# Kernel optimization log

Hardware: AMD Instinct MI355X
Metric: run time of the kernel (lower is better)

Reference implementation:

```python
import jax, jax.numpy as jnp
import numpy as np

DIST_MULT = 0.1
CLIP_LOW = 0.0
EPS = 1e-6


def setup_inputs() -> dict:
    key = jax.random.key(0)
    k1, _ = jax.random.split(key)
    x_msg_binned = jax.random.normal(k1, (8, 64, 512, 16), dtype=jnp.float32)
    msk = jnp.ones((8, 64, 512, 1), dtype=jnp.float32)
    return {"x_msg_binned": x_msg_binned, "msk": msk}


def reference(x_msg_binned, msk):
    # A: (B, bins, N, F) masked node features
    A = x_msg_binned * msk
    na = jnp.sum(A * A, axis=-1)  # (B, bins, N)
    # Gram matrix: (B, bins, N, N)
    G = jnp.einsum("bknf,bkmf->bknm", A, A)
    D = jnp.sqrt(jnp.maximum(na[..., :, None] - 2.0 * G + na[..., None, :], EPS))
    dm = jnp.exp(-DIST_MULT * D)[..., None]  # (B, bins, N, N, 1)
    return jnp.clip(dm, CLIP_LOW, 1.0)
```

## Files before the change

kernel.cpp:

```cpp
#include <hip/hip_runtime.h>


typedef float f32x4 __attribute__((ext_vector_type(4)));

#define NEG_DIST_LOG2E (-0.14426950408889634f)
#define EPS_F 1e-6f
#define LDM 516
#define LDN 68

__global__ __launch_bounds__(512) void node_pair_gaussian_kernel(
    const float* __restrict__ x,
    const float* __restrict__ msk,
    float* __restrict__ out)
{
    __shared__ __align__(16) float lds_m[16][LDM];
    __shared__ __align__(16) float lds_n[16][LDN];
    __shared__ __align__(16) float na_m[512];
    __shared__ __align__(16) float na_n[64];

    const int tid   = threadIdx.x;
    const int slice = blockIdx.x;
    const int r0    = blockIdx.y << 6;

    const float* xs = x   + (size_t)slice * (512 * 16);
    const float* ms = msk + (size_t)slice * 512;

    #pragma unroll
    for (int it = 0; it < 4; ++it) {
        const int c    = tid + it * 512;
        const int node = c >> 2;
        const int f4   = (c & 3) * 4;
        const f32x4 v  = *(const f32x4*)(xs + (size_t)c * 4);
        const float mm = ms[node];
        lds_m[f4 + 0][node] = v.x * mm;
        lds_m[f4 + 1][node] = v.y * mm;
        lds_m[f4 + 2][node] = v.z * mm;
        lds_m[f4 + 3][node] = v.w * mm;
        float p = (v.x * v.x + v.y * v.y + v.z * v.z + v.w * v.w) * (mm * mm);
        p += __shfl_xor(p, 1);
        p += __shfl_xor(p, 2);
        if ((tid & 3) == 0) na_m[node] = p;
    }
    if (tid < 256) {
        const int node = tid >> 2;
        const int f4   = (tid & 3) * 4;
        const f32x4 v  = *(const f32x4*)(xs + (size_t)(r0 + node) * 16 + f4);
        const float mm = ms[r0 + node];
        lds_n[f4 + 0][node] = v.x * mm;
        lds_n[f4 + 1][node] = v.y * mm;
        lds_n[f4 + 2][node] = v.z * mm;
        lds_n[f4 + 3][node] = v.w * mm;
        float p = (v.x * v.x + v.y * v.y + v.z * v.z + v.w * v.w) * (mm * mm);
        p += __shfl_xor(p, 1);
        p += __shfl_xor(p, 2);
        if ((tid & 3) == 0) na_n[node] = p;
    }
    __syncthreads();

    const int lane = tid & 63;
    const int w8   = (tid >> 6) << 3;

    float acc[8][8];
    #pragma unroll
    for (int i = 0; i < 8; ++i)
        #pragma unroll
        for (int j = 0; j < 8; ++j) acc[i][j] = 0.0f;

    #pragma unroll
    for (int f = 0; f < 16; ++f) {
        const f32x4 a0 = *(const f32x4*)&lds_n[f][w8];
        const f32x4 a1 = *(const f32x4*)&lds_n[f][w8 + 4];
        const f32x4 b0 = *(const f32x4*)&lds_m[f][lane * 4];
        const f32x4 b1 = *(const f32x4*)&lds_m[f][256 + lane * 4];
        const float an[8] = {a0.x, a0.y, a0.z, a0.w, a1.x, a1.y, a1.z, a1.w};
        const float am[8] = {b0.x, b0.y, b0.z, b0.w, b1.x, b1.y, b1.z, b1.w};
        #pragma unroll
        for (int i = 0; i < 8; ++i)
            #pragma unroll
            for (int j = 0; j < 8; ++j)
                acc[i][j] = fmaf(an[i], am[j], acc[i][j]);
    }

    const f32x4 nn0 = *(const f32x4*)&na_n[w8];
    const f32x4 nn1 = *(const f32x4*)&na_n[w8 + 4];
    const f32x4 nm0 = *(const f32x4*)&na_m[lane * 4];
    const f32x4 nm1 = *(const f32x4*)&na_m[256 + lane * 4];
    const float nn[8] = {nn0.x, nn0.y, nn0.z, nn0.w, nn1.x, nn1.y, nn1.z, nn1.w};
    const float nm[8] = {nm0.x, nm0.y, nm0.z, nm0.w, nm1.x, nm1.y, nm1.z, nm1.w};

    float* outs = out + (size_t)slice * (512 * 512) + (size_t)r0 * 512;

    #pragma unroll
    for (int i = 0; i < 8; ++i) {
        float r[8];
        #pragma unroll
        for (int j = 0; j < 8; ++j) {
            float s = fmaf(-2.0f, acc[i][j], nn[i] + nm[j]);
            s = fmaxf(s, EPS_F);
            const float d = __builtin_amdgcn_sqrtf(s);
            const float e = __builtin_amdgcn_exp2f(d * NEG_DIST_LOG2E);
            r[j] = fminf(e, 1.0f);
        }
        f32x4 w0 = {r[0], r[1], r[2], r[3]};
        f32x4 w1 = {r[4], r[5], r[6], r[7]};
        float* rowp = outs + (size_t)(w8 + i) * 512;
        __builtin_nontemporal_store(w0, (f32x4*)(rowp + lane * 4));
        __builtin_nontemporal_store(w1, (f32x4*)(rowp + 256 + lane * 4));
    }
}

extern "C" void kernel_launch(void* const* d_in, const int* in_sizes, int n_in,
                              void* d_out, int out_size, void* d_ws, size_t ws_size,
                              hipStream_t stream) {
    const float* x   = (const float*)d_in[0];
    const float* msk = (const float*)d_in[1];
    float* out = (float*)d_out;

    dim3 grid(512, 8);
    node_pair_gaussian_kernel<<<grid, 512, 0, stream>>>(x, msk, out);
}
```

Measured before the change: 525.5 us.

## Process all row tiles per block, reusing one LDS copy of the slice

Each block now handles a whole slice and loops over eight 64-row tiles instead of launching one block per tile. The slice's features and norms are staged in LDS once and read for both row and column operands, so the redundant global loads and the separate row-tile staging go away. The grid shrinks from 4096 to 512 blocks, and a launch-bounds occupancy hint of 4 is added. The kernel is bound by output writes, so the smaller grid and the serial loop could reduce how well stores overlap.

```diff
diff --git a/kernel.cpp b/kernel.cpp
--- a/kernel.cpp
+++ b/kernel.cpp
@@ -6,21 +6,17 @@
 #define NEG_DIST_LOG2E (-0.14426950408889634f)
 #define EPS_F 1e-6f
 #define LDM 516
-#define LDN 68
 
-__global__ __launch_bounds__(512) void node_pair_gaussian_kernel(
+__global__ __launch_bounds__(512, 4) void node_pair_gaussian_kernel(
     const float* __restrict__ x,
     const float* __restrict__ msk,
     float* __restrict__ out)
 {
     __shared__ __align__(16) float lds_m[16][LDM];
-    __shared__ __align__(16) float lds_n[16][LDN];
     __shared__ __align__(16) float na_m[512];
-    __shared__ __align__(16) float na_n[64];
 
     const int tid   = threadIdx.x;
     const int slice = blockIdx.x;
-    const int r0    = blockIdx.y << 6;
 
     const float* xs = x   + (size_t)slice * (512 * 16);
     const float* ms = msk + (size_t)slice * 512;
@@ -41,71 +37,63 @@
         p += __shfl_xor(p, 2);
         if ((tid & 3) == 0) na_m[node] = p;
     }
-    if (tid < 256) {
-        const int node = tid >> 2;
-        const int f4   = (tid & 3) * 4;
-        const f32x4 v  = *(const f32x4*)(xs + (size_t)(r0 + node) * 16 + f4);
-        const float mm = ms[r0 + node];
-        lds_n[f4 + 0][node] = v.x * mm;
-        lds_n[f4 + 1][node] = v.y * mm;
-        lds_n[f4 + 2][node] = v.z * mm;
-        lds_n[f4 + 3][node] = v.w * mm;
-        float p = (v.x * v.x + v.y * v.y + v.z * v.z + v.w * v.w) * (mm * mm);
-        p += __shfl_xor(p, 1);
-        p += __shfl_xor(p, 2);
-        if ((tid & 3) == 0) na_n[node] = p;
-    }
     __syncthreads();
 
     const int lane = tid & 63;
     const int w8   = (tid >> 6) << 3;
 
-    float acc[8][8];
-    #pragma unroll
-    for (int i = 0; i < 8; ++i)
-        #pragma unroll
-        for (int j = 0; j < 8; ++j) acc[i][j] = 0.0f;
+    const f32x4 nm0 = *(const f32x4*)&na_m[lane * 4];
+    const f32x4 nm1 = *(const f32x4*)&na_m[256 + lane * 4];
+    const float nm[8] = {nm0.x, nm0.y, nm0.z, nm0.w, nm1.x, nm1.y, nm1.z, nm1.w};
 
-    #pragma unroll
-    for (int f = 0; f < 16; ++f) {
-        const f32x4 a0 = *(const f32x4*)&lds_n[f][w8];
-        const f32x4 a1 = *(const f32x4*)&lds_n[f][w8 + 4];
-        const f32x4 b0 = *(const f32x4*)&lds_m[f][lane * 4];
-        const f32x4 b1 = *(const f32x4*)&lds_m[f][256 + lane * 4];
-        const float an[8] = {a0.x, a0.y, a0.z, a0.w, a1.x, a1.y, a1.z, a1.w};
-        const float am[8] = {b0.x, b0.y, b0.z, b0.w, b1.x, b1.y, b1.z, b1.w};
+    float* const outs = out + (size_t)slice * (512 * 512);
+
+    for (int r0 = 0; r0 < 512; r0 += 64) {
+        asm volatile("" ::: "memory");
+        const int rb = r0 + w8;
+
+        float acc[8][8];
         #pragma unroll
         for (int i = 0; i < 8; ++i)
             #pragma unroll
-            for (int j = 0; j < 8; ++j)
-                acc[i][j] = fmaf(an[i], am[j], acc[i][j]);
-    }
+            for (int j = 0; j < 8; ++j) acc[i][j] = 0.0f;
 
-    const f32x4 nn0 = *(const f32x4*)&na_n[w8];
-    const f32x4 nn1 = *(const f32x4*)&na_n[w8 + 4];
-    const f32x4 nm0 = *(const f32x4*)&na_m[lane * 4];
-    const f32x4 nm1 = *(const f32x4*)&na_m[256 + lane * 4];
-    const float nn[8] = {nn0.x, nn0.y, nn0.z, nn0.w, nn1.x, nn1.y, nn1.z, nn1.w};
-    const float nm[8] = {nm0.x, nm0.y, nm0.z, nm0.w, nm1.x, nm1.y, nm1.z, nm1.w};
+        #pragma unroll
+        for (int f = 0; f < 16; ++f) {
+            const f32x4 a0 = *(const f32x4*)&lds_m[f][rb];
+            const f32x4 a1 = *(const f32x4*)&lds_m[f][rb + 4];
+            const f32x4 b0 = *(const f32x4*)&lds_m[f][lane * 4];
+            const f32x4 b1 = *(const f32x4*)&lds_m[f][256 + lane * 4];
+            const float an[8] = {a0.x, a0.y, a0.z, a0.w, a1.x, a1.y, a1.z, a1.w};
+            const float am[8] = {b0.x, b0.y, b0.z, b0.w, b1.x, b1.y, b1.z, b1.w};
+            #pragma unroll
+            for (int i = 0; i < 8; ++i)
+                #pragma unroll
+                for (int j = 0; j < 8; ++j)
+                    acc[i][j] = fmaf(an[i], am[j], acc[i][j]);
+        }
 
-    float* outs = out + (size_t)slice * (512 * 512) + (size_t)r0 * 512;
+        const f32x4 nn0 = *(const f32x4*)&na_m[rb];
+        const f32x4 nn1 = *(const f32x4*)&na_m[rb + 4];
+        const float nn[8] = {nn0.x, nn0.y, nn0.z, nn0.w, nn1.x, nn1.y, nn1.z, nn1.w};
 
-    #pragma unroll
-    for (int i = 0; i < 8; ++i) {
-        float r[8];
         #pragma unroll
-        for (int j = 0; j < 8; ++j) {
-            float s = fmaf(-2.0f, acc[i][j], nn[i] + nm[j]);
-            s = fmaxf(s, EPS_F);
-            const float d = __builtin_amdgcn_sqrtf(s);
-            const float e = __builtin_amdgcn_exp2f(d * NEG_DIST_LOG2E);
-            r[j] = fminf(e, 1.0f);
+        for (int i = 0; i < 8; ++i) {
+            float r[8];
+            #pragma unroll
+            for (int j = 0; j < 8; ++j) {
+                float s = fmaf(-2.0f, acc[i][j], nn[i] + nm[j]);
+                s = fmaxf(s, EPS_F);
+                const float d = __builtin_amdgcn_sqrtf(s);
+                const float e = __builtin_amdgcn_exp2f(d * NEG_DIST_LOG2E);
+                r[j] = fminf(e, 1.0f);
+            }
+            f32x4 w0 = {r[0], r[1], r[2], r[3]};
+            f32x4 w1 = {r[4], r[5], r[6], r[7]};
+            float* rowp = outs + (size_t)(rb + i) * 512;
+            __builtin_nontemporal_store(w0, (f32x4*)(rowp + lane * 4));
+            __builtin_nontemporal_store(w1, (f32x4*)(rowp + 256 + lane * 4));
         }
-        f32x4 w0 = {r[0], r[1], r[2], r[3]};
-        f32x4 w1 = {r[4], r[5], r[6], r[7]};
-        float* rowp = outs + (size_t)(w8 + i) * 512;
-        __builtin_nontemporal_store(w0, (f32x4*)(rowp + lane * 4));
-        __builtin_nontemporal_store(w1, (f32x4*)(rowp + 256 + lane * 4));
     }
 }
 
@@ -116,6 +104,6 @@
     const float* msk = (const float*)d_in[1];
     float* out = (float*)d_out;
 
-    dim3 grid(512, 8);
+    dim3 grid(512);
     node_pair_gaussian_kernel<<<grid, 512, 0, stream>>>(x, msk, out);
 }
```

Measured after the change: 546.6 us. 1.04x slower.
